# Optimization experiments

Hardware: AMD Instinct MI355X
Metric: run time of the kernel (lower is better)

Reference implementation:

```python
import jax, jax.numpy as jnp
import numpy as np

VOCAB = 50257
EMB = 1024
H = 1024
LAYERS = 2
B = 64
S = 512


def gru_cell(x, h, w_ih, w_hh, b_ih, b_hh):
    # PyTorch GRUCell math. x:[B,in], h:[B,H], w_ih:[3H,in], w_hh:[3H,H]
    gi = x @ w_ih.T + b_ih            # [B,3H]
    gh = h @ w_hh.T + b_hh            # [B,3H]
    i_r, i_z, i_n = jnp.split(gi, 3, axis=1)
    h_r, h_z, h_n = jnp.split(gh, 3, axis=1)
    r = jax.nn.sigmoid(i_r + h_r)
    z = jax.nn.sigmoid(i_z + h_z)
    n = jnp.tanh(i_n + r * h_n)
    return (1.0 - z) * n + z * h


def setup_inputs() -> dict:
    key = jax.random.key(0)
    ks = jax.random.split(key, 16)
    s = 0.02
    inp = {
        "input_step": jax.random.randint(ks[0], (1, B), 0, VOCAB),
        "last_hidden": jax.random.normal(ks[1], (LAYERS, B, H), jnp.float32),
        "encoder_outputs": jax.random.normal(ks[2], (S, B, H), jnp.float32),
        "emb_table": jax.random.normal(ks[3], (VOCAB, EMB), jnp.float32) * s,
        "w_ih0": jax.random.normal(ks[4], (3 * H, EMB), jnp.float32) * s,
        "w_hh0": jax.random.normal(ks[5], (3 * H, H), jnp.float32) * s,
        "b_ih0": jnp.zeros((3 * H,), jnp.float32),
        "b_hh0": jnp.zeros((3 * H,), jnp.float32),
        "w_ih1": jax.random.normal(ks[6], (3 * H, H), jnp.float32) * s,
        "w_hh1": jax.random.normal(ks[7], (3 * H, H), jnp.float32) * s,
        "b_ih1": jnp.zeros((3 * H,), jnp.float32),
        "b_hh1": jnp.zeros((3 * H,), jnp.float32),
        "concat_w": jax.random.normal(ks[8], (H, 2 * H), jnp.float32) * s,
        "concat_b": jnp.zeros((H,), jnp.float32),
        "out_w": jax.random.normal(ks[9], (VOCAB, H), jnp.float32) * s,
        "out_b": jnp.zeros((VOCAB,), jnp.float32),
    }
    return inp


def reference(input_step, last_hidden, encoder_outputs, emb_table,
              w_ih0, w_hh0, b_ih0, b_hh0, w_ih1, w_hh1, b_ih1, b_hh1,
              concat_w, concat_b, out_w, out_b):
    # embedding (dropout=0 / eval mode)
    x = emb_table[input_step[0]]                       # [B,EMB]
    # 2-layer GRU, single time step
    h0 = gru_cell(x, last_hidden[0], w_ih0, w_hh0, b_ih0, b_hh0)   # [B,H]
    h1 = gru_cell(h0, last_hidden[1], w_ih1, w_hh1, b_ih1, b_hh1)  # [B,H]
    rnn_output = h1                                    # [B,H]
    hidden = jnp.stack([h0, h1], axis=0)               # [LAYERS,B,H]
    # Luong dot attention: scores [S,B] -> softmax over S per batch
    scores = jnp.einsum('bh,sbh->bs', rnn_output, encoder_outputs)  # [B,S]
    attn = jax.nn.softmax(scores, axis=1)              # [B,S]
    context = jnp.einsum('bs,sbh->bh', attn, encoder_outputs)       # [B,H]
    concat_in = jnp.concatenate([rnn_output, context], axis=1)      # [B,2H]
    concat_out = jnp.tanh(concat_in @ concat_w.T + concat_b)        # [B,H]
    logits = concat_out @ out_w.T + out_b              # [B,VOCAB]
    output = jax.nn.softmax(logits, axis=1)
    return (output, hidden)
```

## Files before the change

### kernel.cpp

```cpp
#include <hip/hip_runtime.h>
#include <hip/hip_bf16.h>
#include <math.h>

#define VOCAB 50257
#define EMB   1024
#define HID   1024
#define BATCH 64
#define SEQ   512
#define LOGITS_LD 50304
#define SCH   16
#define NCHUNK (SEQ / SCH)
#define NSLAB 786

typedef __attribute__((ext_vector_type(8))) short bf16x8;
typedef __attribute__((ext_vector_type(4))) float f32x4;

__device__ inline short f2bf(float x) {
    __hip_bfloat16 h = __float2bfloat16(x);
    return *reinterpret_cast<short*>(&h);
}

__device__ inline bf16x8 cvt8(const float4& a, const float4& b) {
    bf16x8 r;
    r[0] = f2bf(a.x); r[1] = f2bf(a.y); r[2] = f2bf(a.z); r[3] = f2bf(a.w);
    r[4] = f2bf(b.x); r[5] = f2bf(b.y); r[6] = f2bf(b.z); r[7] = f2bf(b.w);
    return r;
}

struct Prob {
    const void*  A;
    const int*   gidx;
    const float* W;
    const float* bias;
    float*       C;
    int N, K, ldc;
};

template <int KSLEN, int ADD_BIAS, int A_BF16>
__global__ __launch_bounds__(128, 2) void gemm_k(Prob p0, Prob p1, Prob p2)
{
    Prob P = (blockIdx.y == 0) ? p0 : ((blockIdx.y == 1) ? p1 : p2);

    const int lane = threadIdx.x & 63;
    const int wv   = threadIdx.x >> 6;
    const int rowi = lane & 15;
    const int kgi  = lane >> 4;
    const int col  = blockIdx.x * 32 + wv * 16 + rowi;
    const int wcol = min(col, P.N - 1);
    const int kbase = blockIdx.z * KSLEN + kgi * 8;

    const float* wp = P.W + (size_t)wcol * P.K + kbase;

    const float*  af[4];
    const ushort* ah[4];
#pragma unroll
    for (int mt = 0; mt < 4; ++mt) {
        int r  = rowi + mt * 16;
        int ar = P.gidx ? P.gidx[r] : r;
        af[mt] = (const float*) P.A + (size_t)ar * P.K + kbase;
        ah[mt] = (const ushort*)P.A + (size_t)ar * P.K + kbase;
    }

    f32x4 acc[4] = {};

    float4 wa0, wb0, wa1, wb1;
    bf16x8 h0b[4], h1b[4];
    float4 f0a[4], f0b[4], f1a[4], f1b[4];

    wa0 = *(const float4*)(wp);
    wb0 = *(const float4*)(wp + 4);
#pragma unroll
    for (int mt = 0; mt < 4; ++mt) {
        if (A_BF16) h0b[mt] = *(const bf16x8*)(ah[mt]);
        else { f0a[mt] = *(const float4*)(af[mt]); f0b[mt] = *(const float4*)(af[mt] + 4); }
    }
    wa1 = *(const float4*)(wp + 32);
    wb1 = *(const float4*)(wp + 36);
#pragma unroll
    for (int mt = 0; mt < 4; ++mt) {
        if (A_BF16) h1b[mt] = *(const bf16x8*)(ah[mt] + 32);
        else { f1a[mt] = *(const float4*)(af[mt] + 32); f1b[mt] = *(const float4*)(af[mt] + 36); }
    }

#pragma unroll
    for (int ks = 0; ks < KSLEN; ks += 64) {
        {
            float4 nwa = {}, nwb = {};
            bf16x8 nh[4] = {};
            float4 nfa[4] = {}, nfb[4] = {};
            if (ks + 64 < KSLEN) {
                nwa = *(const float4*)(wp + ks + 64);
                nwb = *(const float4*)(wp + ks + 68);
#pragma unroll
                for (int mt = 0; mt < 4; ++mt) {
                    if (A_BF16) nh[mt] = *(const bf16x8*)(ah[mt] + ks + 64);
                    else { nfa[mt] = *(const float4*)(af[mt] + ks + 64);
                           nfb[mt] = *(const float4*)(af[mt] + ks + 68); }
                }
            }
            bf16x8 b = cvt8(wa0, wb0);
#pragma unroll
            for (int mt = 0; mt < 4; ++mt) {
                bf16x8 a;
                if (A_BF16) a = h0b[mt]; else a = cvt8(f0a[mt], f0b[mt]);
                acc[mt] = __builtin_amdgcn_mfma_f32_16x16x32_bf16(a, b, acc[mt], 0, 0, 0);
            }
            wa0 = nwa; wb0 = nwb;
#pragma unroll
            for (int mt = 0; mt < 4; ++mt) {
                if (A_BF16) h0b[mt] = nh[mt];
                else { f0a[mt] = nfa[mt]; f0b[mt] = nfb[mt]; }
            }
        }
        {
            float4 nwa = {}, nwb = {};
            bf16x8 nh[4] = {};
            float4 nfa[4] = {}, nfb[4] = {};
            if (ks + 96 < KSLEN) {
                nwa = *(const float4*)(wp + ks + 96);
                nwb = *(const float4*)(wp + ks + 100);
#pragma unroll
                for (int mt = 0; mt < 4; ++mt) {
                    if (A_BF16) nh[mt] = *(const bf16x8*)(ah[mt] + ks + 96);
                    else { nfa[mt] = *(const float4*)(af[mt] + ks + 96);
                           nfb[mt] = *(const float4*)(af[mt] + ks + 100); }
                }
            }
            bf16x8 b = cvt8(wa1, wb1);
#pragma unroll
            for (int mt = 0; mt < 4; ++mt) {
                bf16x8 a;
                if (A_BF16) a = h1b[mt]; else a = cvt8(f1a[mt], f1b[mt]);
                acc[mt] = __builtin_amdgcn_mfma_f32_16x16x32_bf16(a, b, acc[mt], 0, 0, 0);
            }
            wa1 = nwa; wb1 = nwb;
#pragma unroll
            for (int mt = 0; mt < 4; ++mt) {
                if (A_BF16) h1b[mt] = nh[mt];
                else { f1a[mt] = nfa[mt]; f1b[mt] = nfb[mt]; }
            }
        }
    }

    if (col < P.N) {
        float bv = ADD_BIAS ? P.bias[col] : 0.0f;
        float* C = P.C + (size_t)blockIdx.z * 64 * P.ldc;
#pragma unroll
        for (int mt = 0; mt < 4; ++mt)
#pragma unroll
            for (int r = 0; r < 4; ++r) {
                int row = mt * 16 + kgi * 4 + r;
                C[(size_t)row * P.ldc + col] = acc[mt][r] + bv;
            }
    }
}

__device__ __forceinline__ void issue_panel(const float* __restrict__ W, int r0,
                                            int p, int tid, float4 (&stg)[16])
{
#pragma unroll
    for (int i = 0; i < 16; ++i) {
        int grow = min(r0 + p * 16 + i, VOCAB - 1);
        stg[i] = *(const float4*)(W + (size_t)grow * 1024 + tid * 4);
    }
}

__device__ __forceinline__ void write_panel(ushort* buf, int tid,
                                            const float4 (&stg)[16])
{
#pragma unroll
    for (int i = 0; i < 16; ++i) {
        unsigned lo = (unsigned)(unsigned short)f2bf(stg[i].x) |
                      ((unsigned)(unsigned short)f2bf(stg[i].y) << 16);
        unsigned hi = (unsigned)(unsigned short)f2bf(stg[i].z) |
                      ((unsigned)(unsigned short)f2bf(stg[i].w) << 16);
        uint2 u = {lo, hi};
        *(uint2*)((char*)buf + i * 2048 + ((tid * 8) ^ ((i & 7) << 4))) = u;
    }
}

__global__ __launch_bounds__(256, 2) void logits_panel_k(
    const ushort* __restrict__ co_bf, const float* __restrict__ W,
    const float* __restrict__ bias, float* __restrict__ logits,
    float* __restrict__ pmax, float* __restrict__ psum, int* __restrict__ ctr)
{
    __shared__ ushort wp_s[2][16 * 1024];
    __shared__ int slab_sh;

    const int tid  = threadIdx.x;
    const int lane = tid & 63;
    const int wv   = tid >> 6;
    const int rowi = lane & 15;
    const int kgi  = lane >> 4;
    const int wswz = (rowi & 7) << 4;

    bf16x8 cob[32];
    {
        const ushort* cp = co_bf + (size_t)(wv * 16 + rowi) * 1024 + kgi * 8;
#pragma unroll
        for (int s = 0; s < 32; ++s)
            cob[s] = *(const bf16x8*)(cp + s * 32);
    }

    while (true) {
        if (tid == 0) slab_sh = atomicAdd(ctr, 1);
        __syncthreads();
        const int slab = slab_sh;
        __syncthreads();
        if (slab >= NSLAB) break;
        const int r0 = slab * 64;

        float4 stg[16];

        issue_panel(W, r0, 0, tid, stg);
        write_panel(wp_s[0], tid, stg);
        issue_panel(W, r0, 1, tid, stg);
        asm volatile("s_waitcnt lgkmcnt(0)" ::: "memory");
        __builtin_amdgcn_s_barrier();

        float m_run = -INFINITY, s_run = 0.0f;

#pragma unroll
        for (int p = 0; p < 4; ++p) {
            f32x4 acc = {};
#pragma unroll
            for (int ks = 0; ks < 32; ++ks) {
                bf16x8 wf = *(const bf16x8*)((const char*)wp_s[p & 1] +
                            rowi * 2048 + ((ks * 64 + kgi * 16) ^ wswz));
                acc = __builtin_amdgcn_mfma_f32_16x16x32_bf16(wf, cob[ks], acc, 0, 0, 0);
            }

            const int vb = r0 + p * 16 + kgi * 4;
            const int bq = wv * 16 + rowi;
            float vals[4];
            if (vb + 3 < VOCAB) {
                float4 bv = *(const float4*)(bias + vb);
                vals[0] = acc[0] + bv.x; vals[1] = acc[1] + bv.y;
                vals[2] = acc[2] + bv.z; vals[3] = acc[3] + bv.w;
            } else {
#pragma unroll
                for (int r = 0; r < 4; ++r)
                    vals[r] = acc[r] + bias[min(vb + r, VOCAB - 1)];
            }
            float4 o = {vals[0], vals[1], vals[2], vals[3]};
            *(float4*)(logits + (size_t)bq * LOGITS_LD + vb) = o;

            float pmv = -INFINITY;
#pragma unroll
            for (int r = 0; r < 4; ++r)
                if (vb + r < VOCAB) pmv = fmaxf(pmv, vals[r]);
            pmv = fmaxf(pmv, __shfl_xor(pmv, 16));
            pmv = fmaxf(pmv, __shfl_xor(pmv, 32));
            float sp = 0.0f;
#pragma unroll
            for (int r = 0; r < 4; ++r)
                if (vb + r < VOCAB) sp += expf(vals[r] - pmv);
            sp += __shfl_xor(sp, 16);
            sp += __shfl_xor(sp, 32);
            float nm = fmaxf(m_run, pmv);
            s_run = s_run * expf(m_run - nm) +
                    ((pmv == -INFINITY) ? 0.0f : sp * expf(pmv - nm));
            m_run = nm;

            if (p < 3) {
                write_panel(wp_s[(p + 1) & 1], tid, stg);
                if (p < 2) issue_panel(W, r0, p + 2, tid, stg);
                asm volatile("s_waitcnt lgkmcnt(0)" ::: "memory");
                __builtin_amdgcn_s_barrier();
            }
        }

        if (kgi == 0) {
            pmax[(size_t)slab * 64 + wv * 16 + rowi] = m_run;
            psum[(size_t)slab * 64 + wv * 16 + rowi] = s_run;
        }
        __syncthreads();
    }
}

__global__ __launch_bounds__(256) void vfinal_k(
    const float* __restrict__ pmax, const float* __restrict__ psum,
    float* __restrict__ gm, float* __restrict__ ginv)
{
    const int b = blockIdx.x;
    __shared__ float red[4];
    float m = -INFINITY;
    for (int s = threadIdx.x; s < NSLAB; s += 256)
        m = fmaxf(m, pmax[(size_t)s * 64 + b]);
    for (int off = 32; off; off >>= 1) m = fmaxf(m, __shfl_xor(m, off));
    int wv = threadIdx.x >> 6, lane = threadIdx.x & 63;
    if (lane == 0) red[wv] = m;
    __syncthreads();
    m = fmaxf(fmaxf(red[0], red[1]), fmaxf(red[2], red[3]));
    float t = 0.0f;
    for (int s = threadIdx.x; s < NSLAB; s += 256)
        t += psum[(size_t)s * 64 + b] * expf(pmax[(size_t)s * 64 + b] - m);
    for (int off = 32; off; off >>= 1) t += __shfl_xor(t, off);
    __syncthreads();
    if (lane == 0) red[wv] = t;
    __syncthreads();
    if (threadIdx.x == 0) { gm[b] = m; ginv[b] = 1.0f / (red[0] + red[1] + red[2] + red[3]); }
}

template <int NZI, int NZH>
__global__ __launch_bounds__(256) void gru_gate_k(
    const float* __restrict__ pgi, const float* __restrict__ pgh,
    const float* __restrict__ b_ih, const float* __restrict__ b_hh,
    const float* __restrict__ hprev, float* __restrict__ out_hidden,
    float* __restrict__ h_out, float* __restrict__ ci)
{
    int i = blockIdx.x * 256 + threadIdx.x;
    int b = i >> 10, j = i & 1023;
    size_t base = (size_t)b * 3072 + j;
    float ir = b_ih[j], iz = b_ih[j + 1024], in_ = b_ih[j + 2048];
    float hr = b_hh[j], hz = b_hh[j + 1024], hn  = b_hh[j + 2048];
#pragma unroll
    for (int z = 0; z < NZI; ++z) {
        size_t o = (size_t)z * 64 * 3072 + base;
        ir += pgi[o]; iz += pgi[o + 1024]; in_ += pgi[o + 2048];
    }
#pragma unroll
    for (int z = 0; z < NZH; ++z) {
        size_t o = (size_t)z * 64 * 3072 + base;
        hr += pgh[o]; hz += pgh[o + 1024]; hn  += pgh[o + 2048];
    }
    float r = 1.0f / (1.0f + expf(-(ir + hr)));
    float z = 1.0f / (1.0f + expf(-(iz + hz)));
    float n = tanhf(in_ + r * hn);
    float v = (1.0f - z) * n + z * hprev[i];
    out_hidden[i] = v;
    if (h_out) h_out[i] = v;
    if (ci)    ci[(size_t)b * 2048 + j] = v;
}

__global__ __launch_bounds__(256) void attn_fused_k(
    const float* __restrict__ h1, const float* __restrict__ enc,
    float* __restrict__ pctx, float* __restrict__ pm, float* __restrict__ ps)
{
    const int b = blockIdx.y, ck = blockIdx.x;
    __shared__ float hs[HID];
    __shared__ float es[SCH][HID];
    __shared__ float sc[SCH];
    const int tid = threadIdx.x, wv = tid >> 6, lane = tid & 63;

    ((float4*)hs)[tid] = ((const float4*)(h1 + (size_t)b * HID))[tid];
    const float* ebase = enc + ((size_t)(ck * SCH) * BATCH + b) * HID;
#pragma unroll
    for (int i = 0; i < SCH; ++i) {
        int idx = tid + i * 256;
        int r = idx >> 8, c = idx & 255;
        ((float4*)es[r])[c] = ((const float4*)(ebase + (size_t)r * BATCH * HID))[c];
    }
    __syncthreads();

#pragma unroll
    for (int i = 0; i < 4; ++i) {
        int r = wv * 4 + i;
        float acc = 0.0f;
#pragma unroll
        for (int seg = 0; seg < 4; ++seg) {
            float4 ev = ((const float4*)es[r])[lane + seg * 64];
            float4 hv = ((const float4*)hs)[lane + seg * 64];
            acc += ev.x * hv.x + ev.y * hv.y + ev.z * hv.z + ev.w * hv.w;
        }
        for (int off = 32; off; off >>= 1) acc += __shfl_down(acc, off);
        if (lane == 0) sc[r] = acc;
    }
    __syncthreads();

    float m = sc[0];
#pragma unroll
    for (int s = 1; s < SCH; ++s) m = fmaxf(m, sc[s]);
    float p[SCH];
    float sum = 0.0f;
#pragma unroll
    for (int s = 0; s < SCH; ++s) { p[s] = expf(sc[s] - m); sum += p[s]; }

    float4 cacc = {0.0f, 0.0f, 0.0f, 0.0f};
#pragma unroll
    for (int s = 0; s < SCH; ++s) {
        float4 ev = ((const float4*)es[s])[tid];
        cacc.x += p[s] * ev.x; cacc.y += p[s] * ev.y;
        cacc.z += p[s] * ev.z; cacc.w += p[s] * ev.w;
    }
    ((float4*)(pctx + ((size_t)ck * BATCH + b) * HID))[tid] = cacc;
    if (tid == 0) { pm[b * NCHUNK + ck] = m; ps[b * NCHUNK + ck] = sum; }
}

__global__ __launch_bounds__(256) void attn_comb_k(
    const float* __restrict__ pctx, const float* __restrict__ pm,
    const float* __restrict__ ps, float* __restrict__ ci)
{
    const int b = blockIdx.x, tid = threadIdx.x;
    float m = -INFINITY;
#pragma unroll
    for (int c = 0; c < NCHUNK; ++c) m = fmaxf(m, pm[b * NCHUNK + c]);
    float w[NCHUNK]; float tot = 0.0f;
#pragma unroll
    for (int c = 0; c < NCHUNK; ++c) {
        w[c] = expf(pm[b * NCHUNK + c] - m);
        tot += ps[b * NCHUNK + c] * w[c];
    }
    float inv = 1.0f / tot;
    float4 acc = {0.0f, 0.0f, 0.0f, 0.0f};
#pragma unroll
    for (int c = 0; c < NCHUNK; ++c) {
        float4 v = ((const float4*)(pctx + ((size_t)c * BATCH + b) * HID))[tid];
        acc.x += w[c] * v.x; acc.y += w[c] * v.y;
        acc.z += w[c] * v.z; acc.w += w[c] * v.w;
    }
    float4 o = {acc.x * inv, acc.y * inv, acc.z * inv, acc.w * inv};
    ((float4*)(ci + (size_t)b * 2048 + 1024))[tid] = o;
}

__global__ __launch_bounds__(256) void concat_comb_k(
    const float* __restrict__ pco, const float* __restrict__ bias,
    ushort* __restrict__ co_bf, int* __restrict__ ctr)
{
    if (blockIdx.x == 0 && threadIdx.x == 0) *ctr = 0;
    int i = blockIdx.x * 256 + threadIdx.x;
    int j = i & 1023;
    float v = bias[j];
#pragma unroll
    for (int z = 0; z < 8; ++z) v += pco[(size_t)z * 65536 + i];
    co_bf[i] = (ushort)f2bf(tanhf(v));
}

__global__ __launch_bounds__(256) void softmax_v_k(
    const float* __restrict__ logits, const float* __restrict__ gm,
    const float* __restrict__ ginv, float* __restrict__ out)
{
    int b = blockIdx.y;
    float m = gm[b], inv = ginv[b];
    int v = blockIdx.x * 1024 + threadIdx.x * 4;
    if (v + 3 < VOCAB) {
        float4 lv = *reinterpret_cast<const float4*>(logits + (size_t)b * LOGITS_LD + v);
        float4 o;
        o.x = expf(lv.x - m) * inv; o.y = expf(lv.y - m) * inv;
        o.z = expf(lv.z - m) * inv; o.w = expf(lv.w - m) * inv;
        *reinterpret_cast<float4*>(out + (size_t)b * VOCAB + v) = o;
    } else {
        for (int k = 0; k < 4 && v + k < VOCAB; ++k)
            out[(size_t)b * VOCAB + v + k] = expf(logits[(size_t)b * LOGITS_LD + v + k] - m) * inv;
    }
}

extern "C" void kernel_launch(void* const* d_in, const int* in_sizes, int n_in,
                              void* d_out, int out_size, void* d_ws, size_t ws_size,
                              hipStream_t stream)
{
    const int*   input_step  = (const int*)  d_in[0];
    const float* last_hidden = (const float*)d_in[1];
    const float* enc         = (const float*)d_in[2];
    const float* emb         = (const float*)d_in[3];
    const float* w_ih0       = (const float*)d_in[4];
    const float* w_hh0       = (const float*)d_in[5];
    const float* b_ih0       = (const float*)d_in[6];
    const float* b_hh0       = (const float*)d_in[7];
    const float* w_ih1       = (const float*)d_in[8];
    const float* w_hh1       = (const float*)d_in[9];
    const float* b_ih1       = (const float*)d_in[10];
    const float* b_hh1       = (const float*)d_in[11];
    const float* concat_w    = (const float*)d_in[12];
    const float* concat_b    = (const float*)d_in[13];
    const float* out_w       = (const float*)d_in[14];
    const float* out_b       = (const float*)d_in[15];

    float* out = (float*)d_out;
    float* out_probs  = out;
    float* out_hidden = out + (size_t)BATCH * VOCAB;

    float* ws   = (float*)d_ws;
    float* big  = ws;
    float* pgi0 = big;
    float* pgh0 = big + 786432;
    float* pgh1 = big + 1572864;
    float* pgi1 = big;
    float* pctx = big;
    float* pco  = big;
    float* logits = ws + 2359296;
    float* ci   = logits + (size_t)64 * LOGITS_LD;
    float* h0   = ci + 131072;
    float* pm   = h0 + 65536;
    float* ps   = pm + 2048;
    float* pmax = ps + 2048;
    float* psum = pmax + 50304;
    float* gm   = psum + 50304;
    float* ginv = gm + 64;
    int*   ctr  = (int*)(ginv + 64);
    ushort* co_bf = (ushort*)(ginv + 64 + 16);

    Prob P0 = { emb,         input_step, w_ih0, nullptr, pgi0, 3 * HID, EMB, 3 * HID };
    Prob P1 = { last_hidden, nullptr,    w_hh0, nullptr, pgh0, 3 * HID, HID, 3 * HID };
    Prob P2 = { last_hidden + 64 * HID, nullptr, w_hh1, nullptr, pgh1, 3 * HID, HID, 3 * HID };

    gemm_k<256, 0, 0><<<dim3(96, 3, 4), 128, 0, stream>>>(P0, P1, P2);

    gru_gate_k<4, 4><<<256, 256, 0, stream>>>(pgi0, pgh0, b_ih0, b_hh0, last_hidden,
                                              out_hidden, h0, nullptr);

    Prob PB = { h0, nullptr, w_ih1, nullptr, pgi1, 3 * HID, HID, 3 * HID };
    gemm_k<128, 0, 0><<<dim3(96, 1, 8), 128, 0, stream>>>(PB, PB, PB);

    gru_gate_k<8, 4><<<256, 256, 0, stream>>>(pgi1, pgh1, b_ih1, b_hh1,
                                              last_hidden + 64 * HID,
                                              out_hidden + 64 * HID, nullptr, ci);

    attn_fused_k<<<dim3(NCHUNK, BATCH), 256, 0, stream>>>(
        out_hidden + 64 * HID, enc, pctx, pm, ps);
    attn_comb_k<<<BATCH, 256, 0, stream>>>(pctx, pm, ps, ci);

    Prob PC = { ci, nullptr, concat_w, nullptr, pco, HID, 2 * HID, HID };
    gemm_k<256, 0, 0><<<dim3(32, 1, 8), 128, 0, stream>>>(PC, PC, PC);
    concat_comb_k<<<256, 256, 0, stream>>>(pco, concat_b, co_bf, ctr);

    logits_panel_k<<<512, 256, 0, stream>>>(co_bf, out_w, out_b, logits, pmax, psum, ctr);

    vfinal_k<<<BATCH, 256, 0, stream>>>(pmax, psum, gm, ginv);
    softmax_v_k<<<dim3((VOCAB + 1023) / 1024, BATCH), 256, 0, stream>>>(
        logits, gm, ginv, out_probs);
}
```

Before: 172.7 us.

## Prefetch next slab across iterations and fuse softmax stats reduction into logits kernel

The persistent logits kernel now grabs the next work slab early and starts loading its first weight panels while the current slab is still being computed. This removes the pipeline drain and refill between slabs. The separate vfinal kernel is replaced by a last-block-done reduction: a second atomic counter picks the final block, which computes the per-batch global max and inverse sum. This saves one kernel launch, at the cost of a serial tail step on a single block and extra fences.

Result: slower. 330.8 us (+91.5%).

```diff
diff --git a/kernel.cpp b/kernel.cpp
--- a/kernel.cpp
+++ b/kernel.cpp
@@ -182,10 +182,12 @@
 __global__ __launch_bounds__(256, 2) void logits_panel_k(
     const ushort* __restrict__ co_bf, const float* __restrict__ W,
     const float* __restrict__ bias, float* __restrict__ logits,
-    float* __restrict__ pmax, float* __restrict__ psum, int* __restrict__ ctr)
+    float* __restrict__ pmax, float* __restrict__ psum,
+    int* __restrict__ ctr, float* __restrict__ gm, float* __restrict__ ginv)
 {
     __shared__ ushort wp_s[2][16 * 1024];
-    __shared__ int slab_sh;
+    __shared__ int slab_sh, rank_sh;
+    __shared__ float fm[4][64], fs[4][64];
 
     const int tid  = threadIdx.x;
     const int lane = tid & 63;
@@ -202,104 +204,119 @@
             cob[s] = *(const bf16x8*)(cp + s * 32);
     }
 
-    while (true) {
-        if (tid == 0) slab_sh = atomicAdd(ctr, 1);
-        __syncthreads();
-        const int slab = slab_sh;
-        __syncthreads();
-        if (slab >= NSLAB) break;
-        const int r0 = slab * 64;
-
+    if (tid == 0) slab_sh = atomicAdd(ctr, 1);
+    __syncthreads();
+    int slab = slab_sh;
+
+    if (slab < NSLAB) {
         float4 stg[16];
-
-        issue_panel(W, r0, 0, tid, stg);
+        issue_panel(W, slab * 64, 0, tid, stg);
         write_panel(wp_s[0], tid, stg);
-        issue_panel(W, r0, 1, tid, stg);
+        issue_panel(W, slab * 64, 1, tid, stg);
         asm volatile("s_waitcnt lgkmcnt(0)" ::: "memory");
         __builtin_amdgcn_s_barrier();
 
-        float m_run = -INFINITY, s_run = 0.0f;
-
-#pragma unroll
-        for (int p = 0; p < 4; ++p) {
-            f32x4 acc = {};
-#pragma unroll
-            for (int ks = 0; ks < 32; ++ks) {
-                bf16x8 wf = *(const bf16x8*)((const char*)wp_s[p & 1] +
-                            rowi * 2048 + ((ks * 64 + kgi * 16) ^ wswz));
-                acc = __builtin_amdgcn_mfma_f32_16x16x32_bf16(wf, cob[ks], acc, 0, 0, 0);
-            }
-
-            const int vb = r0 + p * 16 + kgi * 4;
-            const int bq = wv * 16 + rowi;
-            float vals[4];
-            if (vb + 3 < VOCAB) {
-                float4 bv = *(const float4*)(bias + vb);
-                vals[0] = acc[0] + bv.x; vals[1] = acc[1] + bv.y;
-                vals[2] = acc[2] + bv.z; vals[3] = acc[3] + bv.w;
-            } else {
+        int buf = 0;
+        for (;;) {
+            const int r0 = slab * 64;
+            float m_run = -INFINITY, s_run = 0.0f;
+            int nxt = NSLAB;
+#pragma unroll
+            for (int p = 0; p < 4; ++p) {
+                f32x4 acc = {};
+#pragma unroll
+                for (int ks = 0; ks < 32; ++ks) {
+                    bf16x8 wf = *(const bf16x8*)((const char*)wp_s[buf] +
+                                rowi * 2048 + ((ks * 64 + kgi * 16) ^ wswz));
+                    acc = __builtin_amdgcn_mfma_f32_16x16x32_bf16(wf, cob[ks], acc, 0, 0, 0);
+                }
+                buf ^= 1;
+
+                const int vb = r0 + p * 16 + kgi * 4;
+                const int bq = wv * 16 + rowi;
+                float vals[4];
+                if (vb + 3 < VOCAB) {
+                    float4 bv = *(const float4*)(bias + vb);
+                    vals[0] = acc[0] + bv.x; vals[1] = acc[1] + bv.y;
+                    vals[2] = acc[2] + bv.z; vals[3] = acc[3] + bv.w;
+                } else {
+#pragma unroll
+                    for (int r = 0; r < 4; ++r)
+                        vals[r] = acc[r] + bias[min(vb + r, VOCAB - 1)];
+                }
+                float4 o = {vals[0], vals[1], vals[2], vals[3]};
+                *(float4*)(logits + (size_t)bq * LOGITS_LD + vb) = o;
+
+                float pmv = -INFINITY;
 #pragma unroll
                 for (int r = 0; r < 4; ++r)
-                    vals[r] = acc[r] + bias[min(vb + r, VOCAB - 1)];
-            }
-            float4 o = {vals[0], vals[1], vals[2], vals[3]};
-            *(float4*)(logits + (size_t)bq * LOGITS_LD + vb) = o;
-
-            float pmv = -INFINITY;
-#pragma unroll
-            for (int r = 0; r < 4; ++r)
-                if (vb + r < VOCAB) pmv = fmaxf(pmv, vals[r]);
-            pmv = fmaxf(pmv, __shfl_xor(pmv, 16));
-            pmv = fmaxf(pmv, __shfl_xor(pmv, 32));
-            float sp = 0.0f;
-#pragma unroll
-            for (int r = 0; r < 4; ++r)
-                if (vb + r < VOCAB) sp += expf(vals[r] - pmv);
-            sp += __shfl_xor(sp, 16);
-            sp += __shfl_xor(sp, 32);
-            float nm = fmaxf(m_run, pmv);
-            s_run = s_run * expf(m_run - nm) +
-                    ((pmv == -INFINITY) ? 0.0f : sp * expf(pmv - nm));
-            m_run = nm;
-
-            if (p < 3) {
-                write_panel(wp_s[(p + 1) & 1], tid, stg);
-                if (p < 2) issue_panel(W, r0, p + 2, tid, stg);
+                    if (vb + r < VOCAB) pmv = fmaxf(pmv, vals[r]);
+                pmv = fmaxf(pmv, __shfl_xor(pmv, 16));
+                pmv = fmaxf(pmv, __shfl_xor(pmv, 32));
+                float sp = 0.0f;
+#pragma unroll
+                for (int r = 0; r < 4; ++r)
+                    if (vb + r < VOCAB) sp += expf(vals[r] - pmv);
+                sp += __shfl_xor(sp, 16);
+                sp += __shfl_xor(sp, 32);
+                float nm = fmaxf(m_run, pmv);
+                s_run = s_run * expf(m_run - nm) +
+                        ((pmv == -INFINITY) ? 0.0f : sp * expf(pmv - nm));
+                m_run = nm;
+
+                if (p == 3) {
+                    if (kgi == 0) {
+                        pmax[(size_t)slab * 64 + bq] = m_run;
+                        psum[(size_t)slab * 64 + bq] = s_run;
+                    }
+                    break;
+                }
+
+                write_panel(wp_s[buf], tid, stg);
+                if (p == 0) {
+                    issue_panel(W, r0, 2, tid, stg);
+                } else if (p == 1) {
+                    if (tid == 0) slab_sh = atomicAdd(ctr, 1);
+                    issue_panel(W, r0, 3, tid, stg);
+                } else {
+                    nxt = slab_sh;
+                    if (nxt < NSLAB) issue_panel(W, nxt * 64, 0, tid, stg);
+                }
                 asm volatile("s_waitcnt lgkmcnt(0)" ::: "memory");
                 __builtin_amdgcn_s_barrier();
             }
+
+            if (nxt >= NSLAB) break;
+            write_panel(wp_s[buf], tid, stg);
+            issue_panel(W, nxt * 64, 1, tid, stg);
+            asm volatile("s_waitcnt lgkmcnt(0)" ::: "memory");
+            __builtin_amdgcn_s_barrier();
+            slab = nxt;
         }
-
-        if (kgi == 0) {
-            pmax[(size_t)slab * 64 + wv * 16 + rowi] = m_run;
-            psum[(size_t)slab * 64 + wv * 16 + rowi] = s_run;
+    }
+
+    __threadfence();
+    if (tid == 0) rank_sh = atomicAdd(ctr + 1, 1);
+    __syncthreads();
+    if (rank_sh == (int)gridDim.x - 1) {
+        __threadfence();
+        const int b = tid & 63, q = tid >> 6;
+        float m = -INFINITY;
+        for (int s = q; s < NSLAB; s += 4)
+            m = fmaxf(m, pmax[(size_t)s * 64 + b]);
+        fm[q][b] = m;
+        __syncthreads();
+        m = fmaxf(fmaxf(fm[0][b], fm[1][b]), fmaxf(fm[2][b], fm[3][b]));
+        float t = 0.0f;
+        for (int s = q; s < NSLAB; s += 4)
+            t += psum[(size_t)s * 64 + b] * expf(pmax[(size_t)s * 64 + b] - m);
+        fs[q][b] = t;
+        __syncthreads();
+        if (q == 0) {
+            gm[b]   = m;
+            ginv[b] = 1.0f / (fs[0][b] + fs[1][b] + fs[2][b] + fs[3][b]);
         }
-        __syncthreads();
-    }
-}
-
-__global__ __launch_bounds__(256) void vfinal_k(
-    const float* __restrict__ pmax, const float* __restrict__ psum,
-    float* __restrict__ gm, float* __restrict__ ginv)
-{
-    const int b = blockIdx.x;
-    __shared__ float red[4];
-    float m = -INFINITY;
-    for (int s = threadIdx.x; s < NSLAB; s += 256)
-        m = fmaxf(m, pmax[(size_t)s * 64 + b]);
-    for (int off = 32; off; off >>= 1) m = fmaxf(m, __shfl_xor(m, off));
-    int wv = threadIdx.x >> 6, lane = threadIdx.x & 63;
-    if (lane == 0) red[wv] = m;
-    __syncthreads();
-    m = fmaxf(fmaxf(red[0], red[1]), fmaxf(red[2], red[3]));
-    float t = 0.0f;
-    for (int s = threadIdx.x; s < NSLAB; s += 256)
-        t += psum[(size_t)s * 64 + b] * expf(pmax[(size_t)s * 64 + b] - m);
-    for (int off = 32; off; off >>= 1) t += __shfl_xor(t, off);
-    __syncthreads();
-    if (lane == 0) red[wv] = t;
-    __syncthreads();
-    if (threadIdx.x == 0) { gm[b] = m; ginv[b] = 1.0f / (red[0] + red[1] + red[2] + red[3]); }
+    }
 }
 
 template <int NZI, int NZH>
@@ -417,7 +434,7 @@
     const float* __restrict__ pco, const float* __restrict__ bias,
     ushort* __restrict__ co_bf, int* __restrict__ ctr)
 {
-    if (blockIdx.x == 0 && threadIdx.x == 0) *ctr = 0;
+    if (blockIdx.x == 0 && threadIdx.x < 2) ctr[threadIdx.x] = 0;
     int i = blockIdx.x * 256 + threadIdx.x;
     int j = i & 1023;
     float v = bias[j];
@@ -514,9 +531,9 @@
     gemm_k<256, 0, 0><<<dim3(32, 1, 8), 128, 0, stream>>>(PC, PC, PC);
     concat_comb_k<<<256, 256, 0, stream>>>(pco, concat_b, co_bf, ctr);
 
-    logits_panel_k<<<512, 256, 0, stream>>>(co_bf, out_w, out_b, logits, pmax, psum, ctr);
-
-    vfinal_k<<<BATCH, 256, 0, stream>>>(pmax, psum, gm, ginv);
+    logits_panel_k<<<512, 256, 0, stream>>>(co_bf, out_w, out_b, logits,
+                                            pmax, psum, ctr, gm, ginv);
+
     softmax_v_k<<<dim3((VOCAB + 1023) / 1024, BATCH), 256, 0, stream>>>(
         logits, gm, ginv, out_probs);
 }
```
